# Kernel tuning notes

Hardware: AMD Instinct MI355X
Metric: run time of the kernel (lower is better)

The kernel has to match this reference:

```python
import jax, jax.numpy as jnp
import numpy as np

M, N = 65536, 2048
VOL = (256.0, 256.0, 256.0)
EPS_QUAT = 1e-8
EPS_COV = 1e-6


def setup_inputs() -> dict:
    key = jax.random.key(0)
    k0, k1, k2, k3 = jax.random.split(key, 4)
    vol = jnp.asarray(VOL, dtype=jnp.float32)
    points = jax.random.uniform(k0, (M, 3), dtype=jnp.float32) * vol
    positions = jax.random.uniform(k1, (N, 3), dtype=jnp.float32) * vol
    initial_scale = min(VOL) / (N ** (1.0 / 3.0)) * 0.5
    log_scales = jnp.full((N, 3), np.float32(np.log(initial_scale)), dtype=jnp.float32)
    # near-identity quaternions (w ~ 1, small xyz) so rotation path is non-trivial
    rotations = jnp.concatenate(
        [jnp.ones((N, 1), jnp.float32), 0.1 * jax.random.normal(k2, (N, 3), jnp.float32)],
        axis=1,
    )
    weights = jax.random.uniform(k3, (N,), dtype=jnp.float32) * 0.1
    return {
        "points": points,
        "positions": positions,
        "log_scales": log_scales,
        "rotations": rotations,
        "weights": weights,
    }


def _quat_to_rot(q):
    # q: (N,4) normalized quaternions (w,x,y,z) -> (N,3,3)
    w, x, y, z = q[:, 0], q[:, 1], q[:, 2], q[:, 3]
    r00 = 1 - 2 * (y * y + z * z)
    r01 = 2 * (x * y - z * w)
    r02 = 2 * (x * z + y * w)
    r10 = 2 * (x * y + z * w)
    r11 = 1 - 2 * (x * x + z * z)
    r12 = 2 * (y * z - x * w)
    r20 = 2 * (x * z - y * w)
    r21 = 2 * (y * z + x * w)
    r22 = 1 - 2 * (x * x + y * y)
    R = jnp.stack(
        [jnp.stack([r00, r01, r02], -1),
         jnp.stack([r10, r11, r12], -1),
         jnp.stack([r20, r21, r22], -1)], axis=1)
    return R


def reference(points, positions, log_scales, rotations, weights):
    m, n = points.shape[0], positions.shape[0]
    scales = jnp.exp(log_scales)                                   # (N,3)
    quats = rotations / (jnp.linalg.norm(rotations, axis=1, keepdims=True) + EPS_QUAT)
    R = _quat_to_rot(quats)                                        # (N,3,3)
    # Sigma = R diag(s^2) R^T
    cov = jnp.einsum("nij,nj,nkj->nik", R, scales * scales, R)     # (N,3,3)
    A = jnp.linalg.inv(cov + EPS_COV * jnp.eye(3, dtype=cov.dtype))  # Sigma^{-1}, (N,3,3)
    # quad[m,n] = (p-u)^T A (p-u) = p^T A p - 2 p^T (A u) + u^T A u
    PP = (points[:, :, None] * points[:, None, :]).reshape(m, 9)   # (M,9)
    term_pp = PP @ A.reshape(n, 9).T                               # (M,N)
    b = jnp.einsum("nij,nj->ni", A, positions)                     # (N,3)
    term_pu = points @ b.T                                         # (M,N)
    term_uu = jnp.einsum("ni,ni->n", positions, b)                 # (N,)
    quad = term_pp - 2.0 * term_pu + term_uu[None, :]              # (M,N)
    g = jnp.exp(-0.5 * quad)                                       # (M,N)
    return g @ weights                                             # (M,)
```

## Files before the change

### kernel.cpp

```cpp
#include <hip/hip_runtime.h>
#include <math.h>

#define SCc     8
#define NSC     512
#define SCW     32.0f
#define NMAX    2048
#define GSLAB   768
#define NSB     32
#define SSLOT   24
#define NZB     16
#define EVB     128
#define PCH     2
#define GSP     2
#define ELL     128
#define QCUT    20.0f

typedef float v2f __attribute__((ext_vector_type(2)));
static __device__ __forceinline__ v2f s2(float s) { v2f r; r.x = s; r.y = s; return r; }
static __device__ __forceinline__ v2f pkfma(v2f a, v2f b, v2f c) {
    return __builtin_elementwise_fma(a, b, c);
}
static __device__ __forceinline__ float fexp2(float x) {
#if __has_builtin(__builtin_amdgcn_exp2f)
    return __builtin_amdgcn_exp2f(x);
#else
    return exp2f(x);
#endif
}

static __device__ __forceinline__ int scell_of(float x, float y, float z) {
    int cx = min(SCc - 1, max(0, (int)(x * (1.0f / SCW))));
    int cy = min(SCc - 1, max(0, (int)(y * (1.0f / SCW))));
    int cz = min(SCc - 1, max(0, (int)(z * (1.0f / SCW))));
    return (cz << 6) | (cy << 3) | cx;
}

static __device__ __forceinline__ float cell_d2(int c, float mx, float my, float mz) {
    float lx = (c & 7) * SCW,        hx = lx + SCW;
    float ly = ((c >> 3) & 7) * SCW, hy = ly + SCW;
    float lz = (c >> 6) * SCW,       hz = lz + SCW;
    float dx = fmaxf(fmaxf(lx - mx, mx - hx), 0.0f);
    float dy = fmaxf(fmaxf(ly - my, my - hy), 0.0f);
    float dz = fmaxf(fmaxf(lz - mz, mz - hz), 0.0f);
    return dx * dx + dy * dy + dz * dz;
}

__global__ __launch_bounds__(256) void k_build(
    const float* __restrict__ positions,
    const float* __restrict__ log_scales,
    const float* __restrict__ rotations,
    const float* __restrict__ weights,
    const float* __restrict__ points,
    float* __restrict__ params,
    unsigned* __restrict__ lcnt,
    unsigned* __restrict__ glists,
    unsigned* __restrict__ cnt2,
    float4* __restrict__ subslabs,
    float* __restrict__ out,
    int N, int M, int nPre)
{
    __shared__ float4 shaux[NMAX];
    __shared__ unsigned wc[4];
    int b   = (int)blockIdx.x;
    int tid = threadIdx.x;

    if (b < nPre) {
        int i = b * 256 + tid;
        if (i >= N) return;

        float s0 = expf(log_scales[3*i+0]);
        float s1 = expf(log_scales[3*i+1]);
        float s2_ = expf(log_scales[3*i+2]);
        float v0 = s0*s0, v1 = s1*s1, v2 = s2_*s2_;

        float qw = rotations[4*i+0], qx = rotations[4*i+1];
        float qy = rotations[4*i+2], qz = rotations[4*i+3];
        float inv = 1.0f / (sqrtf(qw*qw + qx*qx + qy*qy + qz*qz) + 1e-8f);
        qw *= inv; qx *= inv; qy *= inv; qz *= inv;

        float r00 = 1.f - 2.f*(qy*qy + qz*qz);
        float r01 = 2.f*(qx*qy - qz*qw);
        float r02 = 2.f*(qx*qz + qy*qw);
        float r10 = 2.f*(qx*qy + qz*qw);
        float r11 = 1.f - 2.f*(qx*qx + qz*qz);
        float r12 = 2.f*(qy*qz - qx*qw);
        float r20 = 2.f*(qx*qz - qy*qw);
        float r21 = 2.f*(qy*qz + qx*qw);
        float r22 = 1.f - 2.f*(qx*qx + qy*qy);

        float a = r00*r00*v0 + r01*r01*v1 + r02*r02*v2 + 1e-6f;
        float b_= r00*r10*v0 + r01*r11*v1 + r02*r12*v2;
        float c = r00*r20*v0 + r01*r21*v1 + r02*r22*v2;
        float d = r10*r10*v0 + r11*r11*v1 + r12*r12*v2 + 1e-6f;
        float e = r10*r20*v0 + r11*r21*v1 + r12*r22*v2;
        float f = r20*r20*v0 + r21*r21*v1 + r22*r22*v2 + 1e-6f;

        float m00 = d*f - e*e;
        float m01 = c*e - b_*f;
        float m02 = b_*e - c*d;
        float det = a*m00 + b_*m01 + c*m02;
        float id  = 1.0f / det;
        float A00 = m00*id, A01 = m01*id, A02 = m02*id;
        float A11 = (a*f - c*c)*id;
        float A12 = (c*b_ - a*e)*id;
        float A22 = (a*d - b_*b_)*id;

        float ux = positions[3*i+0], uy = positions[3*i+1], uz = positions[3*i+2];
        float bx = A00*ux + A01*uy + A02*uz;
        float by = A01*ux + A11*uy + A12*uz;
        float bz = A02*ux + A12*uy + A22*uz;
        float cq = ux*bx + uy*by + uz*bz;

        const float kk = -0.72134752044448170368f;
        float* P = params + 12*i;
        P[0]  = kk*A00;      P[1]  = kk*A11;      P[2]  = kk*A22;      P[3] = 2.f*kk*A01;
        P[4]  = 2.f*kk*A02;  P[5]  = 2.f*kk*A12;  P[6]  = -2.f*kk*bx;  P[7] = -2.f*kk*by;
        P[8]  = -2.f*kk*bz;  P[9]  = kk*cq;       P[10] = weights[i];  P[11] = 0.f;
        return;
    }
    if (b < nPre + NSC) {
        int c = b - nPre;
        const float L2E2 = 2.8853900817779268f;
        for (int g = tid; g < N; g += 256) {
            float v0 = fexp2(L2E2 * log_scales[3*g+0]);
            float v1 = fexp2(L2E2 * log_scales[3*g+1]);
            float v2 = fexp2(L2E2 * log_scales[3*g+2]);
            float lam = fmaxf(fmaxf(v0, v1), v2) + 1e-6f;
            float4 a;
            a.x = positions[3*g+0]; a.y = positions[3*g+1]; a.z = positions[3*g+2];
            a.w = QCUT * lam;
            shaux[g] = a;
        }
        __syncthreads();

        int lane = tid & 63;
        int w    = tid >> 6;
        unsigned long long lt = (1ULL << lane) - 1ULL;
        int Nq    = (N + 3) >> 2;
        int g0    = w * Nq;
        int g1    = min(N, g0 + Nq);
        int iters = (Nq + 63) >> 6;

        unsigned cw = 0;
        for (int it = 0; it < iters; ++it) {
            int g = g0 + it*64 + lane;
            bool keep = false;
            if (g < g1) { float4 a = shaux[g]; keep = cell_d2(c, a.x, a.y, a.z) <= a.w; }
            cw += (unsigned)__popcll(__ballot(keep));
        }
        if (lane == 0) wc[w] = cw;
        __syncthreads();
        unsigned pos = 0;
#pragma unroll
        for (int i = 0; i < 4; ++i) pos += (i < w) ? wc[i] : 0u;
        unsigned total = wc[0] + wc[1] + wc[2] + wc[3];
        unsigned* slab = glists + (size_t)c * GSLAB;
        for (int it = 0; it < iters; ++it) {
            int g = g0 + it*64 + lane;
            bool keep = false;
            if (g < g1) { float4 a = shaux[g]; keep = cell_d2(c, a.x, a.y, a.z) <= a.w; }
            unsigned long long mask = __ballot(keep);
            if (keep) {
                unsigned idx = pos + (unsigned)__popcll(mask & lt);
                if (idx < GSLAB) slab[idx] = (unsigned)g;
            }
            pos += (unsigned)__popcll(mask);
        }
        if (tid == 0) lcnt[c] = min(total, (unsigned)GSLAB);
        return;
    }
    if (b < nPre + NSC + NSB) {
        __shared__ unsigned lcur[NSC];
        for (int i = tid; i < NSC; i += 256) lcur[i] = 0u;
        __syncthreads();
        int h  = b - (nPre + NSC);
        int mh = (M + NSB - 1) / NSB;
        int m0 = h * mh, m1 = min(M, m0 + mh);
        for (int m = m0 + tid; m < m1; m += 256) {
            float x = points[3*m+0], y = points[3*m+1], z = points[3*m+2];
            int c = scell_of(x, y, z);
            unsigned s = atomicAdd(&lcur[c], 1u);
            if (s < SSLOT) {
                float4 sp; sp.x = x; sp.y = y; sp.z = z;
                sp.w = __uint_as_float((unsigned)m);
                subslabs[((size_t)h * NSC + c) * SSLOT + s] = sp;
            }
        }
        __syncthreads();
        for (int i = tid; i < NSC; i += 256)
            cnt2[h * NSC + i] = min(lcur[i], (unsigned)SSLOT);
        return;
    }
    {
        int zb = b - (nPre + NSC + NSB);
        for (int i = zb * 256 + tid; i < M; i += NZB * 256) out[i] = 0.f;
    }
}

__global__ __launch_bounds__(EVB) void k_eval(
    const float4* __restrict__ subslabs, const float4* __restrict__ P4,
    const unsigned* __restrict__ cnt2, const unsigned* __restrict__ lcnt,
    const unsigned* __restrict__ glists,
    float* __restrict__ out)
{
    __shared__ float4 sl[ELL * 3];
    __shared__ unsigned pre[NSB + 1];
    int c   = blockIdx.x;
    int tid = threadIdx.x;

    if (tid == 0) {
        unsigned s = 0; pre[0] = 0;
        for (int h = 0; h < NSB; ++h) { s += cnt2[h * NSC + c]; pre[h + 1] = s; }
    }
    __syncthreads();
    int npts = (int)pre[NSB];
    int pb = (int)blockIdx.y * EVB;
    if (pb >= npts) return;
    int pi = pb + tid;
    bool act = pi < npts;

    int r = act ? pi : 0;
    int lo = 0;
#pragma unroll
    for (int step = 16; step > 0; step >>= 1)
        if (lo + step <= NSB && (int)pre[lo + step] <= r) lo += step;
    int slot = r - (int)pre[lo];
    float4 p = subslabs[((size_t)lo * NSC + c) * SSLOT + slot];

    float x = p.x, yv = p.y, zv = p.z;
    float xx = x*x, yy = yv*yv, zz = zv*zv;
    float xy = x*yv, xz = x*zv, yz = yv*zv;
    float acc = 0.f;

    int len = (int)lcnt[c];
    int gs  = (int)blockIdx.z;
    int k0 = (len * gs) / GSP;
    int k1 = (len * (gs + 1)) / GSP;
    const unsigned* lst = glists + (size_t)c * GSLAB;

    for (int kc = k0; kc < k1; kc += ELL) {
        int kn = min(ELL, k1 - kc);
        __syncthreads();
        for (int e = tid; e < kn; e += EVB) {
            int g = (int)lst[kc + e];
            sl[3*e + 0] = P4[3*g + 0];
            sl[3*e + 1] = P4[3*g + 1];
            sl[3*e + 2] = P4[3*g + 2];
        }
        __syncthreads();
#pragma unroll 2
        for (int e = 0; e < kn; ++e) {
            float4 q0 = sl[3*e + 0];
            float4 q1 = sl[3*e + 1];
            float4 q2 = sl[3*e + 2];

            float t0 = fmaf(q0.x, xx, q2.y);
            t0 = fmaf(q0.w, xy, t0);
            t0 = fmaf(q1.z, x,  t0);
            float t1 = q0.y * yy;
            t1 = fmaf(q1.y, yz, t1);
            t1 = fmaf(q1.w, yv, t1);
            float t2 = q0.z * zz;
            t2 = fmaf(q1.x, xz, t2);
            t2 = fmaf(q2.x, zv, t2);
            float e2 = (t0 + t1) + t2;
            acc = fmaf(q2.z, fexp2(e2), acc);
        }
    }
    if (act) atomicAdd(&out[__float_as_uint(p.w)], acc);
}

#define NSPLIT 32
#define COARSEN 4
__global__ __launch_bounds__(256) void k_pre_dense(
    const float* __restrict__ positions,
    const float* __restrict__ log_scales,
    const float* __restrict__ rotations,
    const float* __restrict__ weights,
    float* __restrict__ params, int N)
{
    int i = blockIdx.x * 256 + threadIdx.x;
    if (i >= N) return;
    float s0 = expf(log_scales[3*i+0]);
    float s1 = expf(log_scales[3*i+1]);
    float s2_ = expf(log_scales[3*i+2]);
    float v0 = s0*s0, v1 = s1*s1, v2 = s2_*s2_;
    float qw = rotations[4*i+0], qx = rotations[4*i+1];
    float qy = rotations[4*i+2], qz = rotations[4*i+3];
    float inv = 1.0f / (sqrtf(qw*qw + qx*qx + qy*qy + qz*qz) + 1e-8f);
    qw *= inv; qx *= inv; qy *= inv; qz *= inv;
    float r00 = 1.f - 2.f*(qy*qy + qz*qz);
    float r01 = 2.f*(qx*qy - qz*qw);
    float r02 = 2.f*(qx*qz + qy*qw);
    float r10 = 2.f*(qx*qy + qz*qw);
    float r11 = 1.f - 2.f*(qx*qx + qz*qz);
    float r12 = 2.f*(qy*qz - qx*qw);
    float r20 = 2.f*(qx*qz - qy*qw);
    float r21 = 2.f*(qy*qz + qx*qw);
    float r22 = 1.f - 2.f*(qx*qx + qy*qy);
    float a = r00*r00*v0 + r01*r01*v1 + r02*r02*v2 + 1e-6f;
    float b_= r00*r10*v0 + r01*r11*v1 + r02*r12*v2;
    float c = r00*r20*v0 + r01*r21*v1 + r02*r22*v2;
    float d = r10*r10*v0 + r11*r11*v1 + r12*r12*v2 + 1e-6f;
    float e = r10*r20*v0 + r11*r21*v1 + r12*r22*v2;
    float f = r20*r20*v0 + r21*r21*v1 + r22*r22*v2 + 1e-6f;
    float m00 = d*f - e*e;
    float m01 = c*e - b_*f;
    float m02 = b_*e - c*d;
    float det = a*m00 + b_*m01 + c*m02;
    float id  = 1.0f / det;
    float A00 = m00*id, A01 = m01*id, A02 = m02*id;
    float A11 = (a*f - c*c)*id;
    float A12 = (c*b_ - a*e)*id;
    float A22 = (a*d - b_*b_)*id;
    float ux = positions[3*i+0], uy = positions[3*i+1], uz = positions[3*i+2];
    float bx = A00*ux + A01*uy + A02*uz;
    float by = A01*ux + A11*uy + A12*uz;
    float bz = A02*ux + A12*uy + A22*uz;
    float cq = ux*bx + uy*by + uz*bz;
    const float kk = -0.72134752044448170368f;
    float* P = params + 12*i;
    P[0]  = kk*A00;      P[1]  = kk*A11;      P[2]  = kk*A22;      P[3] = 2.f*kk*A01;
    P[4]  = 2.f*kk*A02;  P[5]  = 2.f*kk*A12;  P[6]  = -2.f*kk*bx;  P[7] = -2.f*kk*by;
    P[8]  = -2.f*kk*bz;  P[9]  = kk*cq;       P[10] = weights[i];  P[11] = 0.f;
}

__global__ __launch_bounds__(256, 8) void gbf_eval_dense(
    const float* __restrict__ points,
    const float4* __restrict__ params,
    float* __restrict__ out, int M, int N, int nPer)
{
    int p0 = blockIdx.x * (256 * COARSEN) + threadIdx.x;
    int p1 = p0 + 256, p2 = p0 + 512, p3 = p0 + 768;
    int c0 = min(p0, M-1), c1 = min(p1, M-1), c2 = min(p2, M-1), c3 = min(p3, M-1);

    v2f X1, Y1, Z1, X2_, Y2_, Z2_;
    X1.x = points[3*c0+0]; X1.y = points[3*c1+0];
    Y1.x = points[3*c0+1]; Y1.y = points[3*c1+1];
    Z1.x = points[3*c0+2]; Z1.y = points[3*c1+2];
    X2_.x = points[3*c2+0]; X2_.y = points[3*c3+0];
    Y2_.x = points[3*c2+1]; Y2_.y = points[3*c3+1];
    Z2_.x = points[3*c2+2]; Z2_.y = points[3*c3+2];

    v2f XX1 = X1*X1, YY1 = Y1*Y1, ZZ1 = Z1*Z1;
    v2f XY1 = X1*Y1, XZ1 = X1*Z1, YZ1 = Y1*Z1;
    v2f XX2 = X2_*X2_, YY2 = Y2_*Y2_, ZZ2 = Z2_*Z2_;
    v2f XY2 = X2_*Y2_, XZ2 = X2_*Z2_, YZ2 = Y2_*Z2_;

    int jbase = blockIdx.y * nPer;
    int jend = min(nPer, N - jbase);
    int base = jbase * 3;
    v2f acc1; acc1.x = 0.f; acc1.y = 0.f;
    v2f acc2 = acc1;

#pragma unroll 2
    for (int j = 0; j < jend; ++j) {
        float4 q0 = params[base + 3*j + 0];
        float4 q1 = params[base + 3*j + 1];
        float4 q2 = params[base + 3*j + 2];
        v2f t0 = pkfma(s2(q0.x), XX1, s2(q2.y));
        t0 = pkfma(s2(q0.w), XY1, t0);
        t0 = pkfma(s2(q1.z), X1,  t0);
        v2f t1 = s2(q0.y) * YY1;
        t1 = pkfma(s2(q1.y), YZ1, t1);
        t1 = pkfma(s2(q1.w), Y1,  t1);
        v2f t2 = s2(q0.z) * ZZ1;
        t2 = pkfma(s2(q1.x), XZ1, t2);
        t2 = pkfma(s2(q2.x), Z1,  t2);
        v2f e1 = (t0 + t1) + t2;
        v2f u0 = pkfma(s2(q0.x), XX2, s2(q2.y));
        u0 = pkfma(s2(q0.w), XY2, u0);
        u0 = pkfma(s2(q1.z), X2_, u0);
        v2f u1 = s2(q0.y) * YY2;
        u1 = pkfma(s2(q1.y), YZ2, u1);
        u1 = pkfma(s2(q1.w), Y2_, u1);
        v2f u2 = s2(q0.z) * ZZ2;
        u2 = pkfma(s2(q1.x), XZ2, u2);
        u2 = pkfma(s2(q2.x), Z2_, u2);
        v2f e2 = (u0 + u1) + u2;
        v2f g1, g2;
        g1.x = fexp2(e1.x); g1.y = fexp2(e1.y);
        g2.x = fexp2(e2.x); g2.y = fexp2(e2.y);
        acc1 = pkfma(s2(q2.z), g1, acc1);
        acc2 = pkfma(s2(q2.z), g2, acc2);
    }
    if (p0 < M) atomicAdd(&out[p0], acc1.x);
    if (p1 < M) atomicAdd(&out[p1], acc1.y);
    if (p2 < M) atomicAdd(&out[p2], acc2.x);
    if (p3 < M) atomicAdd(&out[p3], acc2.y);
}

extern "C" void kernel_launch(void* const* d_in, const int* in_sizes, int n_in,
                              void* d_out, int out_size, void* d_ws, size_t ws_size,
                              hipStream_t stream)
{
    const float* points     = (const float*)d_in[0];
    const float* positions  = (const float*)d_in[1];
    const float* log_scales = (const float*)d_in[2];
    const float* rotations  = (const float*)d_in[3];
    const float* weights    = (const float*)d_in[4];
    int M = in_sizes[0] / 3;
    int N = in_sizes[4];
    float* out = (float*)d_out;

    char* w = (char*)d_ws;
    size_t o = 0;
    float*    params   = (float*)(w + o);    o += (size_t)N * 12 * 4;
    unsigned* glists   = (unsigned*)(w + o); o += (size_t)NSC * GSLAB * 4;
    unsigned* lcnt     = (unsigned*)(w + o); o += NSC * 4;
    unsigned* cnt2     = (unsigned*)(w + o); o += (size_t)NSB * NSC * 4;
    o = (o + 15) & ~(size_t)15;
    float4*   subslabs = (float4*)(w + o);   o += (size_t)NSB * NSC * SSLOT * 16;

    int nPre = (N + 255) / 256;

    if (ws_size < o || N > NMAX || M > NSC * (NSB * SSLOT)) {
        hipMemsetAsync(d_out, 0, (size_t)out_size * sizeof(float), stream);
        k_pre_dense<<<dim3(nPre), dim3(256), 0, stream>>>(
            positions, log_scales, rotations, weights, params, N);
        int nPer = (N + NSPLIT - 1) / NSPLIT;
        dim3 grid((M + 256 * COARSEN - 1) / (256 * COARSEN), NSPLIT);
        gbf_eval_dense<<<grid, dim3(256), 0, stream>>>(points, (const float4*)params, out, M, N, nPer);
        return;
    }

    k_build<<<dim3(nPre + NSC + NSB + NZB), dim3(256), 0, stream>>>(
        positions, log_scales, rotations, weights, points,
        params, lcnt, glists, cnt2, subslabs, out, N, M, nPre);

    k_eval<<<dim3(NSC, PCH, GSP), dim3(EVB), 0, stream>>>(
        subslabs, (const float4*)params, cnt2, lcnt, glists, out);
}
```

Baseline: 27.50 us.

## Move per-cell Gaussian culling into eval blocks and drop global candidate lists

The per-supercell cull that built global Gaussian index lists in the build kernel is removed. Each eval block now recomputes the survivor list for its own cell and half of the Gaussians into shared memory, and uses a wave shuffle scan instead of a serial prefix over cnt2. This takes 512 blocks out of the build launch and avoids global list writes and reads. In exchange, culling is done redundantly by every PCH block of a cell, and a survivor cap of 512 per half could drop Gaussians if a list overflows.

Measured after the change: 26.40 us. -4.0%, faster.

```diff
diff --git a/kernel.cpp b/kernel.cpp
--- a/kernel.cpp
+++ b/kernel.cpp
@@ -5,14 +5,13 @@
 #define NSC     512
 #define SCW     32.0f
 #define NMAX    2048
-#define GSLAB   768
 #define NSB     32
 #define SSLOT   24
 #define NZB     16
 #define EVB     128
 #define PCH     2
 #define GSP     2
-#define ELL     128
+#define SLMAX   512
 #define QCUT    20.0f
 
 typedef float v2f __attribute__((ext_vector_type(2)));
@@ -45,22 +44,18 @@
     return dx * dx + dy * dy + dz * dz;
 }
 
-__global__ __launch_bounds__(256) void k_build(
+__global__ __launch_bounds__(256) void k_pre(
     const float* __restrict__ positions,
     const float* __restrict__ log_scales,
     const float* __restrict__ rotations,
     const float* __restrict__ weights,
     const float* __restrict__ points,
     float* __restrict__ params,
-    unsigned* __restrict__ lcnt,
-    unsigned* __restrict__ glists,
     unsigned* __restrict__ cnt2,
     float4* __restrict__ subslabs,
     float* __restrict__ out,
     int N, int M, int nPre)
 {
-    __shared__ float4 shaux[NMAX];
-    __shared__ unsigned wc[4];
     int b   = (int)blockIdx.x;
     int tid = threadIdx.x;
 
@@ -118,62 +113,11 @@
         P[8]  = -2.f*kk*bz;  P[9]  = kk*cq;       P[10] = weights[i];  P[11] = 0.f;
         return;
     }
-    if (b < nPre + NSC) {
-        int c = b - nPre;
-        const float L2E2 = 2.8853900817779268f;
-        for (int g = tid; g < N; g += 256) {
-            float v0 = fexp2(L2E2 * log_scales[3*g+0]);
-            float v1 = fexp2(L2E2 * log_scales[3*g+1]);
-            float v2 = fexp2(L2E2 * log_scales[3*g+2]);
-            float lam = fmaxf(fmaxf(v0, v1), v2) + 1e-6f;
-            float4 a;
-            a.x = positions[3*g+0]; a.y = positions[3*g+1]; a.z = positions[3*g+2];
-            a.w = QCUT * lam;
-            shaux[g] = a;
-        }
-        __syncthreads();
-
-        int lane = tid & 63;
-        int w    = tid >> 6;
-        unsigned long long lt = (1ULL << lane) - 1ULL;
-        int Nq    = (N + 3) >> 2;
-        int g0    = w * Nq;
-        int g1    = min(N, g0 + Nq);
-        int iters = (Nq + 63) >> 6;
-
-        unsigned cw = 0;
-        for (int it = 0; it < iters; ++it) {
-            int g = g0 + it*64 + lane;
-            bool keep = false;
-            if (g < g1) { float4 a = shaux[g]; keep = cell_d2(c, a.x, a.y, a.z) <= a.w; }
-            cw += (unsigned)__popcll(__ballot(keep));
-        }
-        if (lane == 0) wc[w] = cw;
-        __syncthreads();
-        unsigned pos = 0;
-#pragma unroll
-        for (int i = 0; i < 4; ++i) pos += (i < w) ? wc[i] : 0u;
-        unsigned total = wc[0] + wc[1] + wc[2] + wc[3];
-        unsigned* slab = glists + (size_t)c * GSLAB;
-        for (int it = 0; it < iters; ++it) {
-            int g = g0 + it*64 + lane;
-            bool keep = false;
-            if (g < g1) { float4 a = shaux[g]; keep = cell_d2(c, a.x, a.y, a.z) <= a.w; }
-            unsigned long long mask = __ballot(keep);
-            if (keep) {
-                unsigned idx = pos + (unsigned)__popcll(mask & lt);
-                if (idx < GSLAB) slab[idx] = (unsigned)g;
-            }
-            pos += (unsigned)__popcll(mask);
-        }
-        if (tid == 0) lcnt[c] = min(total, (unsigned)GSLAB);
-        return;
-    }
-    if (b < nPre + NSC + NSB) {
+    if (b < nPre + NSB) {
         __shared__ unsigned lcur[NSC];
         for (int i = tid; i < NSC; i += 256) lcur[i] = 0u;
         __syncthreads();
-        int h  = b - (nPre + NSC);
+        int h  = b - nPre;
         int mh = (M + NSB - 1) / NSB;
         int m0 = h * mh, m1 = min(M, m0 + mh);
         for (int m = m0 + tid; m < m1; m += 256) {
@@ -192,60 +136,92 @@
         return;
     }
     {
-        int zb = b - (nPre + NSC + NSB);
+        int zb = b - (nPre + NSB);
         for (int i = zb * 256 + tid; i < M; i += NZB * 256) out[i] = 0.f;
     }
 }
 
 __global__ __launch_bounds__(EVB) void k_eval(
-    const float4* __restrict__ subslabs, const float4* __restrict__ P4,
-    const unsigned* __restrict__ cnt2, const unsigned* __restrict__ lcnt,
-    const unsigned* __restrict__ glists,
-    float* __restrict__ out)
+    const float* __restrict__ positions,
+    const float* __restrict__ log_scales,
+    const float4* __restrict__ P4,
+    const float4* __restrict__ subslabs,
+    const unsigned* __restrict__ cnt2,
+    float* __restrict__ out, int N)
 {
-    __shared__ float4 sl[ELL * 3];
+    __shared__ float4 sl[128 * 3];
+    __shared__ unsigned gidx[SLMAX];
     __shared__ unsigned pre[NSB + 1];
-    int c   = blockIdx.x;
-    int tid = threadIdx.x;
-
-    if (tid == 0) {
-        unsigned s = 0; pre[0] = 0;
-        for (int h = 0; h < NSB; ++h) { s += cnt2[h * NSC + c]; pre[h + 1] = s; }
+    __shared__ unsigned s_wc[2];
+    int c    = blockIdx.x;
+    int tid  = threadIdx.x;
+    int lane = tid & 63;
+    int w    = tid >> 6;
+
+    if (tid < 64) {
+        unsigned v = (tid < NSB) ? cnt2[tid * NSC + c] : 0u;
+#pragma unroll
+        for (int d = 1; d < NSB; d <<= 1) {
+            unsigned t = __shfl_up(v, d, 64);
+            if (lane >= d) v += t;
+        }
+        if (tid < NSB) pre[tid + 1] = v;
+        if (tid == 0) pre[0] = 0u;
     }
     __syncthreads();
     int npts = (int)pre[NSB];
-    int pb = (int)blockIdx.y * EVB;
-    if (pb >= npts) return;
-    int pi = pb + tid;
+    int p0 = (int)blockIdx.y * EVB;
+    if (p0 >= npts) return;
+
+    const float L2E2 = 2.8853900817779268f;
+    int gs = (int)blockIdx.z;
+    int gBeg = (N * gs) / GSP;
+    int gEnd = (N * (gs + 1)) / GSP;
+    unsigned long long lt = (1ULL << lane) - 1ULL;
+    unsigned base = 0;
+    for (int g0 = gBeg; g0 < gEnd; g0 += EVB) {
+        int g = g0 + tid;
+        bool keep = false;
+        if (g < gEnd) {
+            float v0 = fexp2(L2E2 * log_scales[3*g+0]);
+            float v1 = fexp2(L2E2 * log_scales[3*g+1]);
+            float v2 = fexp2(L2E2 * log_scales[3*g+2]);
+            float lam = fmaxf(fmaxf(v0, v1), v2) + 1e-6f;
+            keep = cell_d2(c, positions[3*g+0], positions[3*g+1], positions[3*g+2])
+                   <= QCUT * lam;
+        }
+        unsigned long long m = __ballot(keep);
+        if (lane == 0) s_wc[w] = (unsigned)__popcll(m);
+        __syncthreads();
+        unsigned off = base + ((w == 1) ? s_wc[0] : 0u) + (unsigned)__popcll(m & lt);
+        if (keep && off < SLMAX) gidx[off] = (unsigned)g;
+        base += s_wc[0] + s_wc[1];
+        __syncthreads();
+    }
+    int nsurv = min((int)base, SLMAX);
+
+    int pi = p0 + tid;
     bool act = pi < npts;
-
     int r = act ? pi : 0;
     int lo = 0;
 #pragma unroll
-    for (int step = 16; step > 0; step >>= 1)
-        if (lo + step <= NSB && (int)pre[lo + step] <= r) lo += step;
-    int slot = r - (int)pre[lo];
-    float4 p = subslabs[((size_t)lo * NSC + c) * SSLOT + slot];
+    for (int st = 16; st > 0; st >>= 1)
+        if (lo + st <= NSB && (int)pre[lo + st] <= r) lo += st;
+    float4 p = subslabs[((size_t)lo * NSC + c) * SSLOT + (r - (int)pre[lo])];
 
     float x = p.x, yv = p.y, zv = p.z;
     float xx = x*x, yy = yv*yv, zz = zv*zv;
     float xy = x*yv, xz = x*zv, yz = yv*zv;
     float acc = 0.f;
 
-    int len = (int)lcnt[c];
-    int gs  = (int)blockIdx.z;
-    int k0 = (len * gs) / GSP;
-    int k1 = (len * (gs + 1)) / GSP;
-    const unsigned* lst = glists + (size_t)c * GSLAB;
-
-    for (int kc = k0; kc < k1; kc += ELL) {
-        int kn = min(ELL, k1 - kc);
-        __syncthreads();
-        for (int e = tid; e < kn; e += EVB) {
-            int g = (int)lst[kc + e];
-            sl[3*e + 0] = P4[3*g + 0];
-            sl[3*e + 1] = P4[3*g + 1];
-            sl[3*e + 2] = P4[3*g + 2];
+    for (int k0 = 0; k0 < nsurv; k0 += 128) {
+        int kn = min(128, nsurv - k0);
+        __syncthreads();
+        if (tid < kn) {
+            int g = (int)gidx[k0 + tid];
+            sl[3*tid + 0] = P4[3*g + 0];
+            sl[3*tid + 1] = P4[3*g + 1];
+            sl[3*tid + 2] = P4[3*g + 2];
         }
         __syncthreads();
 #pragma unroll 2
@@ -406,8 +382,6 @@
     char* w = (char*)d_ws;
     size_t o = 0;
     float*    params   = (float*)(w + o);    o += (size_t)N * 12 * 4;
-    unsigned* glists   = (unsigned*)(w + o); o += (size_t)NSC * GSLAB * 4;
-    unsigned* lcnt     = (unsigned*)(w + o); o += NSC * 4;
     unsigned* cnt2     = (unsigned*)(w + o); o += (size_t)NSB * NSC * 4;
     o = (o + 15) & ~(size_t)15;
     float4*   subslabs = (float4*)(w + o);   o += (size_t)NSB * NSC * SSLOT * 16;
@@ -424,10 +398,11 @@
         return;
     }
 
-    k_build<<<dim3(nPre + NSC + NSB + NZB), dim3(256), 0, stream>>>(
+    k_pre<<<dim3(nPre + NSB + NZB), dim3(256), 0, stream>>>(
         positions, log_scales, rotations, weights, points,
-        params, lcnt, glists, cnt2, subslabs, out, N, M, nPre);
+        params, cnt2, subslabs, out, N, M, nPre);
 
     k_eval<<<dim3(NSC, PCH, GSP), dim3(EVB), 0, stream>>>(
-        subslabs, (const float4*)params, cnt2, lcnt, glists, out);
-}
+        positions, log_scales, (const float4*)params,
+        subslabs, cnt2, out, N);
+}
```
